# Optimization experiments

Hardware: AMD Instinct MI355X
Metric: run time of the kernel (lower is better)

The kernel has to match this reference:

```python
import jax, jax.numpy as jnp
import numpy as np


def _cayley(X):
    # torch orthogonal parametrization, orthogonal_map='cayley', use_trivialization=False:
    # A = tril(X,-1); A = A - A^T (skew);  Q = (I - A/2)^{-1} (I + A/2)
    n = X.shape[0]
    A = jnp.tril(X, -1)
    A = A - A.T
    I = jnp.eye(n, dtype=X.dtype)
    return jnp.linalg.solve(I - 0.5 * A, I + 0.5 * A)


def setup_inputs() -> dict:
    key = jax.random.key(0)
    ks = jax.random.split(key, 8)
    L, R = 64, 64
    B, S = 4, 2048
    x = jax.random.normal(ks[0], (B, S, L * R), dtype=jnp.float32)
    return {
        "x": x,
        "u_left": jax.random.normal(ks[1], (L, L), dtype=jnp.float32) * 0.02,
        "v_left": jax.random.normal(ks[2], (L, L), dtype=jnp.float32) * 0.02,
        "diag_left": jnp.ones((L,), dtype=jnp.float32),
        "u_right": jax.random.normal(ks[3], (R, R), dtype=jnp.float32) * 0.02,
        "v_right": jax.random.normal(ks[4], (R, R), dtype=jnp.float32) * 0.02,
        "diag_right": jnp.ones((R,), dtype=jnp.float32),
        "diag_scale": 1.0 + 0.01 * jax.random.normal(ks[5], (L * R,), dtype=jnp.float32),
    }


def reference(x, u_left, v_left, diag_left, u_right, v_right, diag_right, diag_scale):
    L = diag_left.shape[0]
    R = diag_right.shape[0]
    # SVD-composed trans matrices: M = Cayley(U) @ diag(S) @ Cayley(V)
    m_left = _cayley(u_left) @ (diag_left[:, None] * _cayley(v_left))    # [L, L]
    m_right = _cayley(u_right) @ (diag_right[:, None] * _cayley(v_right))  # [R, R]
    # add_diag: elementwise diagonal scale on hidden dim
    xs = x * diag_scale
    shp = xs.shape
    xm = xs.reshape(-1, L, R)  # [N, L, R]
    # kronecker_matmul: m_left^T @ X @ m_right
    out = jnp.einsum('il,nij,jr->nlr', m_left, xm, m_right)
    return out.reshape(shp)
```

## Files before the change

### kernel.cpp

```cpp
#include <hip/hip_runtime.h>
#include <hip/hip_bf16.h>

typedef __attribute__((ext_vector_type(8))) short short8;
typedef __attribute__((ext_vector_type(4))) short short4v;
typedef __attribute__((ext_vector_type(4))) float floatx4;

#define MFMA(a, b, c) __builtin_amdgcn_mfma_f32_16x16x32_bf16((a), (b), (c), 0, 0, 0)

__device__ __forceinline__ short f2bf(float f) {
    unsigned u = __float_as_uint(f);
    u += 0x7fffu + ((u >> 16) & 1u);
    return (short)(u >> 16);
}

__device__ __forceinline__ short8 pack_bf16(floatx4 a, floatx4 b) {
    short8 r;
    r[0] = f2bf(a.x); r[1] = f2bf(a.y); r[2] = f2bf(a.z); r[3] = f2bf(a.w);
    r[4] = f2bf(b.x); r[5] = f2bf(b.y); r[6] = f2bf(b.z); r[7] = f2bf(b.w);
    return r;
}

__device__ void cayley64(const float* __restrict__ X, const float* __restrict__ dg,
                         short* outArr, int mode,
                         short* Brow, float* Bcol, short* T0, short* T1, int tid)
{
    int i0 = (tid * 16) >> 6;
    int j0 = (tid * 16) & 63;
#pragma unroll
    for (int s = 0; s < 16; ++s) {
        int i = i0, j = j0 + s;
        float b = 0.f;
        if (i > j)      b =  0.5f * X[i * 64 + j];
        else if (i < j) b = -0.5f * X[j * 64 + i];
        Brow[i * 72 + j] = f2bf(b);
        Bcol[j * 68 + i] = b;
        T0[j * 72 + i]   = f2bf(b);
    }
    __syncthreads();

    int lane = tid & 63, w = tid >> 6, m = lane & 15, q = lane >> 4;
    int arow = (w * 16 + m) * 72;
    short8 a0 = *(const short8*)&Brow[arow + q * 8];
    short8 a1 = *(const short8*)&Brow[arow + 32 + q * 8];

    short* Tbuf[2] = {T0, T1};
    int cur = 0;
    const int NSTEP = 6;
    for (int step = 0; step < NSTEP; ++step) {
        bool last = (step == NSTEP - 1);
        short* Tr = Tbuf[cur];
        short* Tw = Tbuf[cur ^ 1];
#pragma unroll
        for (int c = 0; c < 4; ++c) {
            int coff = c * 16 + m;
            short8 b0 = *(const short8*)&Tr[coff * 72 + q * 8];
            short8 b1 = *(const short8*)&Tr[coff * 72 + 32 + q * 8];
            floatx4 acc = {0.f, 0.f, 0.f, 0.f};
            acc = MFMA(a0, b0, acc);
            acc = MFMA(a1, b1, acc);
            int row0 = w * 16 + q * 4;
            floatx4 badd = *(const floatx4*)&Bcol[coff * 68 + row0];
            floatx4 t = badd + acc;
            if (!last) {
                short4v pk = { f2bf(t.x), f2bf(t.y), f2bf(t.z), f2bf(t.w) };
                *(short4v*)&Tw[coff * 72 + row0] = pk;
            } else {
                int col = coff;
                floatx4 cv;
                cv.x = ((row0 + 0) == col ? 1.f : 0.f) + 2.f * t.x;
                cv.y = ((row0 + 1) == col ? 1.f : 0.f) + 2.f * t.y;
                cv.z = ((row0 + 2) == col ? 1.f : 0.f) + 2.f * t.z;
                cv.w = ((row0 + 3) == col ? 1.f : 0.f) + 2.f * t.w;
                if (mode == 0) {
                    outArr[(row0 + 0) * 72 + col] = f2bf(cv.x);
                    outArr[(row0 + 1) * 72 + col] = f2bf(cv.y);
                    outArr[(row0 + 2) * 72 + col] = f2bf(cv.z);
                    outArr[(row0 + 3) * 72 + col] = f2bf(cv.w);
                } else {
                    floatx4 dv = *(const floatx4*)&dg[row0];
                    short4v pk = { f2bf(cv.x * dv.x), f2bf(cv.y * dv.y),
                                   f2bf(cv.z * dv.z), f2bf(cv.w * dv.w) };
                    *(short4v*)&outArr[col * 72 + row0] = pk;
                }
            }
        }
        __syncthreads();
        cur ^= 1;
    }
}

__global__ __launch_bounds__(256) void k_prep(
        const float* __restrict__ u_l, const float* __restrict__ v_l, const float* __restrict__ dg_l,
        const float* __restrict__ u_r, const float* __restrict__ v_r, const float* __restrict__ dg_r,
        short* __restrict__ wsOut)
{
    __shared__ __align__(16) short Brow[64 * 72];
    __shared__ __align__(16) float Bcol[64 * 68];
    __shared__ __align__(16) short T0[64 * 72];
    __shared__ __align__(16) short T1[64 * 72];
    __shared__ __align__(16) short CvA[64 * 72];
    __shared__ __align__(16) short CuB[64 * 72];

    int tid = threadIdx.x;
    const float* U  = (blockIdx.x == 0) ? u_l  : u_r;
    const float* V  = (blockIdx.x == 0) ? v_l  : v_r;
    const float* DG = (blockIdx.x == 0) ? dg_l : dg_r;
    short* outT = wsOut + blockIdx.x * 4096;

    cayley64(V, DG, CvA, 1, Brow, Bcol, T0, T1, tid);
    __syncthreads();
    cayley64(U, DG, CuB, 0, Brow, Bcol, T0, T1, tid);
    __syncthreads();

    int lane = tid & 63, w = tid >> 6, m = lane & 15, q = lane >> 4;
    int arow = (w * 16 + m) * 72;
    short8 a0 = *(const short8*)&CvA[arow + q * 8];
    short8 a1 = *(const short8*)&CvA[arow + 32 + q * 8];
#pragma unroll
    for (int c = 0; c < 4; ++c) {
        short8 b0 = *(const short8*)&CuB[(c * 16 + m) * 72 + q * 8];
        short8 b1 = *(const short8*)&CuB[(c * 16 + m) * 72 + 32 + q * 8];
        floatx4 acc = {0.f, 0.f, 0.f, 0.f};
        acc = MFMA(a0, b0, acc);
        acc = MFMA(a1, b1, acc);
        int row0 = w * 16 + q * 4, col = c * 16 + m;
        outT[(row0 + 0) * 64 + col] = f2bf(acc.x);
        outT[(row0 + 1) * 64 + col] = f2bf(acc.y);
        outT[(row0 + 2) * 64 + col] = f2bf(acc.z);
        outT[(row0 + 3) * 64 + col] = f2bf(acc.w);
    }
}

__global__ __launch_bounds__(256, 3) void k_main(
        const float* __restrict__ x, const float* __restrict__ dsc,
        const short* __restrict__ mLT, const short* __restrict__ mRT,
        float* __restrict__ out, int N)
{
    __shared__ __align__(16) char  STb[4][8192];
    __shared__ __align__(16) float dsl[64 * 68];

    const int tid = threadIdx.x;
    const int w = tid >> 6, lane = tid & 63, m = lane & 15, q = lane >> 4;
    const int s8 = m & 7;
    char* st = STb[w];

    {
        int row = tid >> 2, c4 = (tid & 3) * 16;
        const float* g = dsc + row * 64 + c4;
        float* l = dsl + row * 68 + c4;
        *(floatx4*)&l[0]  = *(const floatx4*)&g[0];
        *(floatx4*)&l[4]  = *(const floatx4*)&g[4];
        *(floatx4*)&l[8]  = *(const floatx4*)&g[8];
        *(floatx4*)&l[12] = *(const floatx4*)&g[12];
    }

    short8 pf[4][2], qf[4][2];
#pragma unroll
    for (int r = 0; r < 4; ++r) {
        pf[r][0] = *(const short8*)&mLT[(r * 16 + m) * 64 + q * 8];
        pf[r][1] = *(const short8*)&mLT[(r * 16 + m) * 64 + 32 + q * 8];
        qf[r][0] = *(const short8*)&mRT[(r * 16 + m) * 64 + q * 8];
        qf[r][1] = *(const short8*)&mRT[(r * 16 + m) * 64 + 32 + q * 8];
    }
    __syncthreads();

    const long stride = (long)gridDim.x * 4;
    const long wgid = (long)blockIdx.x * 4 + w;
    if (wgid >= N) return;

    const int loff = m * 64 + q * 8;

#define LDCHUNK(p, j, r0, r1, r2, r3) do {                       \
        const float* cp_ = (p) + (j) * 1024;                     \
        r0 = *(const floatx4*)&cp_[0];                           \
        r1 = *(const floatx4*)&cp_[4];                           \
        r2 = *(const floatx4*)&cp_[32];                          \
        r3 = *(const floatx4*)&cp_[36];                          \
        asm volatile("" ::: "memory");     \
    } while (0)

#define PHASE_A(rt, r0, r1, r2, r3) do {                                      \
        const float* dp_ = &dsl[((rt) * 16 + m) * 68 + q * 8];                \
        floatx4 d0_ = *(const floatx4*)&dp_[0];                               \
        floatx4 d1_ = *(const floatx4*)&dp_[4];                               \
        floatx4 d2_ = *(const floatx4*)&dp_[32];                              \
        floatx4 d3_ = *(const floatx4*)&dp_[36];                              \
        short8 a0_ = pack_bf16(r0 * d0_, r1 * d1_);             \
        short8 a1_ = pack_bf16(r2 * d2_, r3 * d3_);             \
        _Pragma("unroll")                                                     \
        for (int c_ = 0; c_ < 4; ++c_) {                                      \
            floatx4 s_ = {0.f, 0.f, 0.f, 0.f};                                \
            s_ = MFMA(a0_, qf[c_][0], s_);                                    \
            s_ = MFMA(a1_, qf[c_][1], s_);                                    \
            short4v pk_ = { f2bf(s_.x), f2bf(s_.y), f2bf(s_.z), f2bf(s_.w) }; \
            *(short4v*)&st[(c_ * 16 + m) * 128 +                              \
                (((2 * (rt) + (q >> 1)) ^ s8) << 4) + (q & 1) * 8] = pk_;     \
        }                                                                     \
    } while (0)

    long n = wgid;
    const float* xp = x + n * 4096 + loff;

    floatx4 A0, A1, A2, A3, B0, B1, B2, B3, C0, C1, C2, C3, D0, D1, D2, D3;
    LDCHUNK(xp, 0, A0, A1, A2, A3);
    LDCHUNK(xp, 1, B0, B1, B2, B3);

    for (;;) {
        const long nn = n + stride;
        const bool hasnext = (nn < N);

        LDCHUNK(xp, 2, C0, C1, C2, C3);
        PHASE_A(0, A0, A1, A2, A3);
        LDCHUNK(xp, 3, D0, D1, D2, D3);
        PHASE_A(1, B0, B1, B2, B3);
        if (hasnext) {
            const float* xn = xp + stride * 4096;
            LDCHUNK(xn, 0, A0, A1, A2, A3);
            PHASE_A(2, C0, C1, C2, C3);
            LDCHUNK(xn, 1, B0, B1, B2, B3);
            PHASE_A(3, D0, D1, D2, D3);
        } else {
            PHASE_A(2, C0, C1, C2, C3);
            PHASE_A(3, D0, D1, D2, D3);
        }

        float* op = out + (size_t)n * 4096;
#pragma unroll
        for (int c2 = 0; c2 < 4; ++c2) {
            const int rowb = (c2 * 16 + m) * 128;
            short8 sb0 = *(const short8*)&st[rowb + ((q       ^ s8) << 4)];
            short8 sb1 = *(const short8*)&st[rowb + (((4 + q) ^ s8) << 4)];
#pragma unroll
            for (int r = 0; r < 4; ++r) {
                floatx4 o = {0.f, 0.f, 0.f, 0.f};
                o = MFMA(sb0, pf[r][0], o);
                o = MFMA(sb1, pf[r][1], o);
                *(floatx4*)&op[(r * 16 + m) * 64 + c2 * 16 + q * 4] = o;
            }
        }

        if (!hasnext) break;
        n = nn;
        xp += stride * 4096;
    }
#undef LDCHUNK
#undef PHASE_A
}

extern "C" void kernel_launch(void* const* d_in, const int* in_sizes, int n_in,
                              void* d_out, int out_size, void* d_ws, size_t ws_size,
                              hipStream_t stream) {
    const float* x    = (const float*)d_in[0];
    const float* u_l  = (const float*)d_in[1];
    const float* v_l  = (const float*)d_in[2];
    const float* dg_l = (const float*)d_in[3];
    const float* u_r  = (const float*)d_in[4];
    const float* v_r  = (const float*)d_in[5];
    const float* dg_r = (const float*)d_in[6];
    const float* dsc  = (const float*)d_in[7];
    float* out = (float*)d_out;
    short* ws  = (short*)d_ws;

    int N = in_sizes[0] / 4096;

    hipLaunchKernelGGL(k_prep, dim3(2), dim3(256), 0, stream,
                       u_l, v_l, dg_l, u_r, v_r, dg_r, ws);
    hipLaunchKernelGGL(k_main, dim3(768), dim3(256), 0, stream,
                       x, dsc, ws, ws + 4096, out, N);
}
```

Baseline: 283.6 us.

## Restructure main loop to prefetch whole next tile during second GEMM stage

Replaces the staggered two-chunk-ahead load schedule with one batch of sixteen vector loads for the entire next 64x64 tile. The batch is issued after the first MFMA stage so it overlaps the second MFMA stage and the output stores. The second stage now interleaves two column blocks per iteration, and occupancy drops from 3 to 2 blocks per CU with the grid shrinking from 768 to 512. This is meant to raise memory-level parallelism and give load latency more cover, at the cost of more registers and fewer resident waves.

```diff
diff --git a/kernel.cpp b/kernel.cpp
--- a/kernel.cpp
+++ b/kernel.cpp
@@ -131,7 +131,7 @@
     }
 }
 
-__global__ __launch_bounds__(256, 3) void k_main(
+__global__ __launch_bounds__(256, 2) void k_main(
         const float* __restrict__ x, const float* __restrict__ dsc,
         const short* __restrict__ mLT, const short* __restrict__ mRT,
         float* __restrict__ out, int N)
@@ -170,13 +170,20 @@
 
     const int loff = m * 64 + q * 8;
 
-#define LDCHUNK(p, j, r0, r1, r2, r3) do {                       \
-        const float* cp_ = (p) + (j) * 1024;                     \
-        r0 = *(const floatx4*)&cp_[0];                           \
-        r1 = *(const floatx4*)&cp_[4];                           \
-        r2 = *(const floatx4*)&cp_[32];                          \
-        r3 = *(const floatx4*)&cp_[36];                          \
-        asm volatile("" ::: "memory");     \
+#define LD16(p) do {                                                     \
+        const float* b0_ = (p);                                          \
+        x00 = *(const floatx4*)&b0_[0];    x01 = *(const floatx4*)&b0_[4];    \
+        x02 = *(const floatx4*)&b0_[32];   x03 = *(const floatx4*)&b0_[36];   \
+        const float* b1_ = (p) + 1024;                                   \
+        x10 = *(const floatx4*)&b1_[0];    x11 = *(const floatx4*)&b1_[4];    \
+        x12 = *(const floatx4*)&b1_[32];   x13 = *(const floatx4*)&b1_[36];   \
+        const float* b2_ = (p) + 2048;                                   \
+        x20 = *(const floatx4*)&b2_[0];    x21 = *(const floatx4*)&b2_[4];    \
+        x22 = *(const floatx4*)&b2_[32];   x23 = *(const floatx4*)&b2_[36];   \
+        const float* b3_ = (p) + 3072;                                   \
+        x30 = *(const floatx4*)&b3_[0];    x31 = *(const floatx4*)&b3_[4];    \
+        x32 = *(const floatx4*)&b3_[32];   x33 = *(const floatx4*)&b3_[36];   \
+        asm volatile("" ::: "memory");                                   \
     } while (0)
 
 #define PHASE_A(rt, r0, r1, r2, r3) do {                                      \
@@ -201,49 +208,53 @@
     long n = wgid;
     const float* xp = x + n * 4096 + loff;
 
-    floatx4 A0, A1, A2, A3, B0, B1, B2, B3, C0, C1, C2, C3, D0, D1, D2, D3;
-    LDCHUNK(xp, 0, A0, A1, A2, A3);
-    LDCHUNK(xp, 1, B0, B1, B2, B3);
+    floatx4 x00, x01, x02, x03, x10, x11, x12, x13;
+    floatx4 x20, x21, x22, x23, x30, x31, x32, x33;
+
+    LD16(xp);
 
     for (;;) {
         const long nn = n + stride;
         const bool hasnext = (nn < N);
 
-        LDCHUNK(xp, 2, C0, C1, C2, C3);
-        PHASE_A(0, A0, A1, A2, A3);
-        LDCHUNK(xp, 3, D0, D1, D2, D3);
-        PHASE_A(1, B0, B1, B2, B3);
-        if (hasnext) {
-            const float* xn = xp + stride * 4096;
-            LDCHUNK(xn, 0, A0, A1, A2, A3);
-            PHASE_A(2, C0, C1, C2, C3);
-            LDCHUNK(xn, 1, B0, B1, B2, B3);
-            PHASE_A(3, D0, D1, D2, D3);
-        } else {
-            PHASE_A(2, C0, C1, C2, C3);
-            PHASE_A(3, D0, D1, D2, D3);
-        }
+        PHASE_A(0, x00, x01, x02, x03);
+        PHASE_A(1, x10, x11, x12, x13);
+        PHASE_A(2, x20, x21, x22, x23);
+        PHASE_A(3, x30, x31, x32, x33);
+        asm volatile("" ::: "memory");
+
+        const float* xnp = xp + (size_t)stride * 4096;
+        if (hasnext) LD16(xnp);
+        asm volatile("" ::: "memory");
 
         float* op = out + (size_t)n * 4096;
 #pragma unroll
-        for (int c2 = 0; c2 < 4; ++c2) {
-            const int rowb = (c2 * 16 + m) * 128;
-            short8 sb0 = *(const short8*)&st[rowb + ((q       ^ s8) << 4)];
-            short8 sb1 = *(const short8*)&st[rowb + (((4 + q) ^ s8) << 4)];
+        for (int cp = 0; cp < 2; ++cp) {
+            const int rowbA = ((2 * cp) * 16 + m) * 128;
+            const int rowbB = ((2 * cp + 1) * 16 + m) * 128;
+            short8 sbA0 = *(const short8*)&st[rowbA + ((q       ^ s8) << 4)];
+            short8 sbA1 = *(const short8*)&st[rowbA + (((4 + q) ^ s8) << 4)];
+            short8 sbB0 = *(const short8*)&st[rowbB + ((q       ^ s8) << 4)];
+            short8 sbB1 = *(const short8*)&st[rowbB + (((4 + q) ^ s8) << 4)];
 #pragma unroll
             for (int r = 0; r < 4; ++r) {
-                floatx4 o = {0.f, 0.f, 0.f, 0.f};
-                o = MFMA(sb0, pf[r][0], o);
-                o = MFMA(sb1, pf[r][1], o);
-                *(floatx4*)&op[(r * 16 + m) * 64 + c2 * 16 + q * 4] = o;
+                floatx4 oa = {0.f, 0.f, 0.f, 0.f};
+                floatx4 ob = {0.f, 0.f, 0.f, 0.f};
+                oa = MFMA(sbA0, pf[r][0], oa);
+                oa = MFMA(sbA1, pf[r][1], oa);
+                ob = MFMA(sbB0, pf[r][0], ob);
+                ob = MFMA(sbB1, pf[r][1], ob);
+                float* rp = &op[(r * 16 + m) * 64];
+                *(floatx4*)&rp[(2 * cp) * 16 + q * 4]     = oa;
+                *(floatx4*)&rp[(2 * cp + 1) * 16 + q * 4] = ob;
             }
         }
 
         if (!hasnext) break;
         n = nn;
-        xp += stride * 4096;
-    }
-#undef LDCHUNK
+        xp = xnp;
+    }
+#undef LD16
 #undef PHASE_A
 }
 
@@ -265,6 +276,6 @@
 
     hipLaunchKernelGGL(k_prep, dim3(2), dim3(256), 0, stream,
                        u_l, v_l, dg_l, u_r, v_r, dg_r, ws);
-    hipLaunchKernelGGL(k_main, dim3(768), dim3(256), 0, stream,
+    hipLaunchKernelGGL(k_main, dim3(512), dim3(256), 0, stream,
                        x, dsc, ws, ws + 4096, out, N);
 }
```

Result: faster. 270.2 us (-4.7%).
